# Optimization experiments

Hardware: AMD Instinct MI355X
Metric: run time of the kernel (lower is better)

## Reference

```python
import jax, jax.numpy as jnp
import numpy as np

N = 20000          # total nodes across batched graphs
E_REL = 60000      # edges per relation type (3 relation types)
N_CLASSES = 32
NUM_GRAPHS = 64
HEADS = 8
OUT_CH = 48
FUSED = 384        # 3 * 128 fused node feature dim
EPS = 1e-5         # PyG LayerNorm eps
NEG_SLOPE = 0.2    # RGATConv leaky_relu slope
NUM_ITERS = 2


def setup_inputs() -> dict:
    key = jax.random.key(0)
    ks = iter(jax.random.split(key, 48))

    def nrm(shape, scale=0.05):
        return jax.random.normal(next(ks), shape, jnp.float32) * scale

    inp = {}
    inp["x_visual"] = jax.random.normal(next(ks), (N, 1024), jnp.float32)
    inp["x_geom"] = jax.random.normal(next(ks), (N, 6), jnp.float32)
    inp["x_prior"] = jax.random.uniform(next(ks), (N, N_CLASSES + 1), jnp.float32)
    inp["edge_index_overlap"] = jax.random.randint(next(ks), (2, E_REL), 0, N)
    inp["edge_index_arch"] = jax.random.randint(next(ks), (2, E_REL), 0, N)
    inp["edge_index_spatial"] = jax.random.randint(next(ks), (2, E_REL), 0, N)
    inp["batch"] = jnp.sort(jax.random.randint(next(ks), (N,), 0, NUM_GRAPHS))
    # encoders: Linear -> ReLU -> PyG LayerNorm(graph mode, batch=None)
    inp["vis_W"] = nrm((1024, 128)); inp["vis_b"] = jnp.zeros((128,), jnp.float32)
    inp["vis_lnw"] = jnp.ones((128,), jnp.float32); inp["vis_lnb"] = jnp.zeros((128,), jnp.float32)
    inp["geo_W"] = nrm((6, 128)); inp["geo_b"] = jnp.zeros((128,), jnp.float32)
    inp["geo_lnw"] = jnp.ones((128,), jnp.float32); inp["geo_lnb"] = jnp.zeros((128,), jnp.float32)
    inp["pri_W"] = nrm((N_CLASSES + 1, 128)); inp["pri_b"] = jnp.zeros((128,), jnp.float32)
    inp["pri_lnw"] = jnp.ones((128,), jnp.float32); inp["pri_lnb"] = jnp.zeros((128,), jnp.float32)
    # RGATConv params: weight (R, in, H*O), q/k (H*O, H*dim) with dim=1, bias (H*O)
    for i in (1, 2):
        inp[f"rgat{i}_W"] = nrm((3, FUSED, HEADS * OUT_CH))
        inp[f"rgat{i}_q"] = nrm((HEADS * OUT_CH, HEADS))
        inp[f"rgat{i}_k"] = nrm((HEADS * OUT_CH, HEADS))
        inp[f"rgat{i}_bias"] = jnp.zeros((HEADS * OUT_CH,), jnp.float32)
        inp[f"n{i}_w"] = jnp.ones((FUSED,), jnp.float32)
        inp[f"n{i}_b"] = jnp.zeros((FUSED,), jnp.float32)
    inp["cls_W1"] = nrm((FUSED, 128)); inp["cls_b1"] = jnp.zeros((128,), jnp.float32)
    inp["cls_W2"] = nrm((128, N_CLASSES)); inp["cls_b2"] = jnp.zeros((N_CLASSES,), jnp.float32)
    return inp


def _encoder(x, W, b, lnw, lnb):
    # Linear -> ReLU -> PyG LayerNorm(mode='graph', batch=None): scalar mean/std
    h = jax.nn.relu(x @ W + b)
    h = h - h.mean()
    h = h / (h.std() + EPS)
    return h * lnw + lnb


def _graph_layernorm(x, batch, w, b):
    # PyG LayerNorm(mode='graph') with batch vector: normalize per graph over nodes*channels
    cnt = jax.ops.segment_sum(jnp.ones((x.shape[0],), x.dtype), batch, NUM_GRAPHS)
    norm = jnp.clip(cnt, 1.0, None) * x.shape[-1]
    mean = jax.ops.segment_sum(x, batch, NUM_GRAPHS).sum(-1) / norm
    xc = x - mean[batch][:, None]
    var = jax.ops.segment_sum(xc * xc, batch, NUM_GRAPHS).sum(-1) / norm
    out = xc / jnp.sqrt(var + EPS)[batch][:, None]
    return out * w + b


def _rgat(x, src, dst, etype, W, q, k, bias):
    # RGATConv: additive self-attention, across-relation softmax, concat heads, sum aggr
    n = x.shape[0]
    xr = jnp.einsum('nf,rfo->rno', x, W)          # per-relation node transform (R,N,H*O)
    outi = xr[etype, dst]                          # (E, H*O) transformed dst features
    outj = xr[etype, src]                          # (E, H*O) transformed src features
    alpha = jax.nn.leaky_relu(outi @ q + outj @ k, NEG_SLOPE)  # (E, H)
    amax = jax.ops.segment_max(alpha, dst, n)
    amax = jnp.where(jnp.isfinite(amax), amax, 0.0)
    ex = jnp.exp(alpha - amax[dst])
    den = jax.ops.segment_sum(ex, dst, n)
    a = ex / (den[dst] + 1e-16)                    # per-dst-node softmax over all relations
    msg = (a[:, :, None] * outj.reshape(-1, HEADS, OUT_CH)).reshape(-1, HEADS * OUT_CH)
    return jax.ops.segment_sum(msg, dst, n) + bias


def reference(x_visual, x_geom, x_prior, edge_index_overlap, edge_index_arch,
              edge_index_spatial, batch, vis_W, vis_b, vis_lnw, vis_lnb,
              geo_W, geo_b, geo_lnw, geo_lnb, pri_W, pri_b, pri_lnw, pri_lnb,
              rgat1_W, rgat1_q, rgat1_k, rgat1_bias, n1_w, n1_b,
              rgat2_W, rgat2_q, rgat2_k, rgat2_bias, n2_w, n2_b,
              cls_W1, cls_b1, cls_W2, cls_b2):
    ei = jnp.concatenate([edge_index_overlap, edge_index_arch, edge_index_spatial], axis=1)
    src, dst = ei[0], ei[1]
    etype = jnp.concatenate([jnp.full((E_REL,), r, jnp.int32) for r in range(3)])

    h_vis = _encoder(x_visual, vis_W, vis_b, vis_lnw, vis_lnb)
    h_geo = _encoder(x_geom, geo_W, geo_b, geo_lnw, geo_lnb)

    cur_prior = x_prior
    logits = None
    for t in range(NUM_ITERS):
        h_pri = _encoder(cur_prior, pri_W, pri_b, pri_lnw, pri_lnb)
        h0 = jnp.concatenate([h_vis, h_geo, h_pri], axis=-1)  # (N, 384)
        h1 = jax.nn.elu(_rgat(h0, src, dst, etype, rgat1_W, rgat1_q, rgat1_k, rgat1_bias)) + h0
        h1 = _graph_layernorm(h1, batch, n1_w, n1_b)
        h2 = jax.nn.elu(_rgat(h1, src, dst, etype, rgat2_W, rgat2_q, rgat2_k, rgat2_bias)) + h1
        h2 = _graph_layernorm(h2, batch, n2_w, n2_b)
        logits = jax.nn.relu(h2 @ cls_W1 + cls_b1) @ cls_W2 + cls_b2  # dropout off (eval)
        if t < NUM_ITERS - 1:
            probs = jax.nn.softmax(logits, axis=-1)
            cur_prior = jnp.concatenate([probs, probs.max(-1, keepdims=True)], axis=-1)
    return logits
```

## Files before the change

kernel.cpp:

```cpp
#include <hip/hip_runtime.h>
#include <hip/hip_bf16.h>

#define Nn 20000
#define EREL 60000
#define ETOT 180000
#define NG 64
#define FD 384
#define EPS 1e-5f

typedef unsigned short u16;
typedef unsigned int u32;
typedef __attribute__((ext_vector_type(8))) short s8v;
typedef __attribute__((ext_vector_type(4))) float f4v;

static inline int cdiv(int a, int b) { return (a + b - 1) / b; }

__device__ inline u16 f2b(float f) {
    __hip_bfloat16 h = __float2bfloat16(f);
    union { __hip_bfloat16 b; u16 u; } c; c.b = h; return c.u;
}
__device__ inline float b2f(u16 u) {
    union { __hip_bfloat16 b; u16 u; } c; c.u = u; return __bfloat162float(c.b);
}

template<bool WLO>
__global__ void tsplit_k(const float* __restrict__ W, u16* __restrict__ hi,
                         u16* __restrict__ lo, int K, int N, int total)
{
    int idx = blockIdx.x * 256 + threadIdx.x;
    if (idx >= total) return;
    int kn = K * N;
    int b = idx / kn, rem = idx - b * kn;
    int k = rem / N, n = rem - k * N;
    float v = W[idx];
    u16 h = f2b(v);
    int o = b * kn + n * K + k;
    hi[o] = h;
    if (WLO) lo[o] = f2b(v - b2f(h));
}

__global__ __launch_bounds__(256) void w2_k(const float* __restrict__ W0,
    const float* __restrict__ q0, const float* __restrict__ k0,
    const float* __restrict__ W1, const float* __restrict__ q1, const float* __restrict__ k1,
    u16* __restrict__ hi, u16* __restrict__ lo)
{
    int row = blockIdx.x * 4 + (threadIdx.x >> 6);
    int lane = threadIdx.x & 63;
    if (row >= 2304) return;
    int kin = row % 384;
    int lr3 = row / 384;
    int L = lr3 / 3, r = lr3 - L * 3;
    const float* W = (L ? W1 : W0) + ((size_t)r * 384 + kin) * 384;
    const float* qm = L ? q1 : q0;
    const float* km = L ? k1 : k0;
    float pq[16] = {};
    #pragma unroll
    for (int j = 0; j < 6; j++) {
        int d = lane + 64 * j;
        float x = W[d];
        #pragma unroll
        for (int h = 0; h < 8; h++) {
            pq[h]     = fmaf(x, qm[d * 8 + h], pq[h]);
            pq[8 + h] = fmaf(x, km[d * 8 + h], pq[8 + h]);
        }
    }
    #pragma unroll
    for (int o = 32; o; o >>= 1) {
        #pragma unroll
        for (int h = 0; h < 16; h++) pq[h] += __shfl_down(pq[h], o);
    }
    if (lane == 0) {
        #pragma unroll
        for (int c = 0; c < 16; c++) {
            u16 hh = f2b(pq[c]);
            size_t o = ((size_t)L * 48 + r * 16 + c) * 384 + kin;
            hi[o] = hh; lo[o] = f2b(pq[c] - b2f(hh));
        }
    }
}

__global__ __launch_bounds__(256) void enc_gemm_k(const float* __restrict__ x, int K,
    const float* __restrict__ W, const float* __restrict__ bias,
    u16* __restrict__ out, float* __restrict__ stats)
{
    __shared__ float Wl[33 * 128];
    __shared__ float bl[128];
    __shared__ float red[8];
    int t = threadIdx.x;
    for (int i = t; i < K * 128; i += 256) Wl[i] = W[i];
    if (t < 128) bl[t] = bias[t];
    __syncthreads();
    int wid = t >> 6, lane = t & 63;
    float s1 = 0.f, s2 = 0.f;
    for (int rr = 0; rr < 8; rr++) {
        int n = blockIdx.x * 32 + wid * 8 + rr;
        if (n >= Nn) break;
        float xv = (lane < K) ? x[(size_t)n * K + lane] : 0.f;
        float a0 = 0.f, a1 = 0.f;
        for (int k = 0; k < K; k++) {
            float xk = __shfl(xv, k);
            a0 = fmaf(xk, Wl[k * 128 + 2 * lane], a0);
            a1 = fmaf(xk, Wl[k * 128 + 2 * lane + 1], a1);
        }
        a0 = fmaxf(a0 + bl[2 * lane], 0.f);
        a1 = fmaxf(a1 + bl[2 * lane + 1], 0.f);
        ((u32*)(out + (size_t)n * FD))[lane] = (u32)f2b(a0) | ((u32)f2b(a1) << 16);
        s1 += a0 + a1; s2 += a0 * a0 + a1 * a1;
    }
    #pragma unroll
    for (int o = 32; o; o >>= 1) { s1 += __shfl_down(s1, o); s2 += __shfl_down(s2, o); }
    if (lane == 0) { red[wid] = s1; red[4 + wid] = s2; }
    __syncthreads();
    if (t == 0) atomicAdd(&stats[0], red[0] + red[1] + red[2] + red[3]);
    if (t == 1) atomicAdd(&stats[1], red[4] + red[5] + red[6] + red[7]);
}

#define USEI(i) ((i) < 2 || ((i) >= 4 && (i) < 6) || (TERMS >= 2 && ((i) == 2 || (i) == 3)) || (TERMS >= 3 && (i) >= 6))
template<bool BIAS, bool RELU, bool STATS, bool OB16, int TERMS, bool SWZ, bool AF32>
__global__ __launch_bounds__(256) void mgemm_k(
    const u16* __restrict__ Ahi, const u16* __restrict__ Alo, const float* __restrict__ Af,
    const u16* __restrict__ Bhi, const u16* __restrict__ Blo,
    const float* __restrict__ bias, void* __restrict__ Cv,
    int M, int K, int ldc, int bstride, float* __restrict__ stats)
{
    __shared__ u16 lds[4 * 128 * 32];
    __shared__ float red[256];
    const int t = threadIdx.x;
    int brow, bcol, z;
    if (SWZ) {
        int d = blockIdx.x;
        int xcd = d & 7, s = d >> 3;
        int row = xcd + 8 * (s / 9);
        int c = s % 9;
        brow = row * 128;
        if (brow >= M) return;
        bcol = (c % 3) * 128;
        z = c / 3;
    } else {
        brow = blockIdx.x * 128; bcol = blockIdx.y * 128; z = blockIdx.z;
    }
    Bhi += (size_t)z * bstride;
    Blo += (size_t)z * bstride;
    float* Cf = OB16 ? nullptr : (float*)Cv + (size_t)z * M * ldc;
    u16*   Ch = OB16 ? (u16*)Cv + (size_t)z * M * ldc : nullptr;

    const int r0 = t >> 2, sl = t & 3;
    const int rA0 = min(brow + r0, M - 1);
    const int rA1 = min(brow + r0 + 64, M - 1);
    const u16* gsrc[8];
    gsrc[0] = Ahi + (size_t)rA0 * K + sl * 8;
    gsrc[1] = Ahi + (size_t)rA1 * K + sl * 8;
    gsrc[2] = Alo + (size_t)rA0 * K + sl * 8;
    gsrc[3] = Alo + (size_t)rA1 * K + sl * 8;
    gsrc[4] = Bhi + (size_t)(bcol + r0) * K + sl * 8;
    gsrc[5] = Bhi + (size_t)(bcol + r0 + 64) * K + sl * 8;
    gsrc[6] = Blo + (size_t)(bcol + r0) * K + sl * 8;
    gsrc[7] = Blo + (size_t)(bcol + r0 + 64) * K + sl * 8;
    const float* afsrc[2];
    if (AF32) {
        afsrc[0] = Af + (size_t)rA0 * K + sl * 8;
        afsrc[1] = Af + (size_t)rA1 * K + sl * 8;
    }
    const int swz = (sl ^ (r0 & 3)) << 3;
    int ldst[8];
    #pragma unroll
    for (int i = 0; i < 8; i++) {
        int tile = i >> 1, row = r0 + 64 * (i & 1);
        ldst[i] = tile * 4096 + row * 32 + swz;
    }

    const int l = t & 63, w = t >> 6;
    const int wr = (w >> 1) * 64, wc = (w & 1) * 64;
    const int lr = l & 15, kq = l >> 4;

    f4v acc[4][4] = {};
    const int NK = K >> 5;

    #define LDA32(i, ko) ({ \
        float4 f0_ = *(const float4*)(afsrc[i] + (ko)); \
        float4 f1_ = *(const float4*)(afsrc[i] + (ko) + 4); \
        s8v r_; \
        r_[0] = (short)f2b(f0_.x); r_[1] = (short)f2b(f0_.y); \
        r_[2] = (short)f2b(f0_.z); r_[3] = (short)f2b(f0_.w); \
        r_[4] = (short)f2b(f1_.x); r_[5] = (short)f2b(f1_.y); \
        r_[6] = (short)f2b(f1_.z); r_[7] = (short)f2b(f1_.w); \
        r_; })

    s8v stg[8];
    #pragma unroll
    for (int i = 0; i < 8; i++) {
        if (AF32 && i < 2) stg[i] = LDA32(i, 0);
        else if (!(AF32 && i < 2) && USEI(i)) stg[i] = *(const s8v*)gsrc[i];
    }

    for (int kc = 0; kc < NK; kc++) {
        if (kc) __syncthreads();
        #pragma unroll
        for (int i = 0; i < 8; i++) if (USEI(i)) *(s8v*)(lds + ldst[i]) = stg[i];
        __syncthreads();
        if (kc + 1 < NK) {
            const int ko = (kc + 1) * 32;
            #pragma unroll
            for (int i = 0; i < 8; i++) {
                if (AF32 && i < 2) stg[i] = LDA32(i, ko);
                else if (!(AF32 && i < 2) && USEI(i)) stg[i] = *(const s8v*)(gsrc[i] + ko);
            }
        }
        #define LDR(T, row) (*(const s8v*)(lds + (T) * 4096 + (row) * 32 + ((kq ^ ((row) & 3)) << 3)))
        s8v bh[4], bl[4];
        #pragma unroll
        for (int tn = 0; tn < 4; tn++) {
            int rb = wc + tn * 16 + lr;
            bh[tn] = LDR(2, rb);
            if (TERMS >= 3) bl[tn] = LDR(3, rb);
        }
        #pragma unroll
        for (int tm = 0; tm < 4; tm++) {
            int ra = wr + tm * 16 + lr;
            s8v ah = LDR(0, ra);
            s8v al;
            if (TERMS >= 2) al = LDR(1, ra);
            #pragma unroll
            for (int tn = 0; tn < 4; tn++) {
                acc[tm][tn] = __builtin_amdgcn_mfma_f32_16x16x32_bf16(ah, bh[tn], acc[tm][tn], 0, 0, 0);
                if (TERMS >= 2)
                    acc[tm][tn] = __builtin_amdgcn_mfma_f32_16x16x32_bf16(al, bh[tn], acc[tm][tn], 0, 0, 0);
                if (TERMS >= 3)
                    acc[tm][tn] = __builtin_amdgcn_mfma_f32_16x16x32_bf16(ah, bl[tn], acc[tm][tn], 0, 0, 0);
            }
        }
        #undef LDR
    }
    #undef LDA32

    float s1 = 0.f, s2 = 0.f;
    #pragma unroll
    for (int tm = 0; tm < 4; tm++) {
        #pragma unroll
        for (int rg = 0; rg < 4; rg++) {
            int row = brow + wr + tm * 16 + kq * 4 + rg;
            if (row < M) {
                #pragma unroll
                for (int tn = 0; tn < 4; tn++) {
                    int col = bcol + wc + tn * 16 + lr;
                    float v = acc[tm][tn][rg];
                    if (BIAS) v += bias[col];
                    if (RELU) v = fmaxf(v, 0.f);
                    if (OB16) Ch[(size_t)row * ldc + col] = f2b(v);
                    else      Cf[(size_t)row * ldc + col] = v;
                    if (STATS) { s1 += v; s2 += v * v; }
                }
            }
        }
    }
    if (STATS) {
        __syncthreads();
        red[t] = s1; __syncthreads();
        for (int o = 128; o; o >>= 1) { if (t < o) red[t] += red[t + o]; __syncthreads(); }
        if (t == 0) atomicAdd(&stats[0], red[0]);
        __syncthreads();
        red[t] = s2; __syncthreads();
        for (int o = 128; o; o >>= 1) { if (t < o) red[t] += red[t + o]; __syncthreads(); }
        if (t == 0) atomicAdd(&stats[1], red[0]);
    }
}
#undef USEI

__global__ __launch_bounds__(256) void projh_k(const u16* __restrict__ hs,
    const u16* __restrict__ w2hi, const u16* __restrict__ w2lo, float* __restrict__ qik)
{
    __shared__ u16 a_lds[128 * 32];
    __shared__ u16 b_lds[2][48 * 392];
    int t = threadIdx.x;
    int brow = blockIdx.x * 128;

    for (int i = t; i < 2304; i += 256) {
        int col = i / 48, c8 = (i - col * 48) * 8;
        *(s8v*)&b_lds[0][col * 392 + c8] = *(const s8v*)(w2hi + col * 384 + c8);
        *(s8v*)&b_lds[1][col * 392 + c8] = *(const s8v*)(w2lo + col * 384 + c8);
    }

    int ar = t >> 1, sl0 = (t & 1) * 2;
    int grow = min(brow + ar, Nn - 1);
    const u16* asrc = hs + (size_t)grow * FD;
    int adst0 = ar * 32 + ((sl0 ^ (ar & 3)) << 3);
    int adst1 = ar * 32 + (((sl0 + 1) ^ (ar & 3)) << 3);

    int l = t & 63, w = t >> 6;
    int lr = l & 15, kq = l >> 4;
    f4v acc[2][3] = {};

    s8v stg0 = *(const s8v*)(asrc + sl0 * 8);
    s8v stg1 = *(const s8v*)(asrc + sl0 * 8 + 8);
    for (int kc = 0; kc < 12; kc++) {
        if (kc) __syncthreads();
        *(s8v*)&a_lds[adst0] = stg0;
        *(s8v*)&a_lds[adst1] = stg1;
        __syncthreads();
        if (kc + 1 < 12) {
            int ko = (kc + 1) * 32 + sl0 * 8;
            stg0 = *(const s8v*)(asrc + ko);
            stg1 = *(const s8v*)(asrc + ko + 8);
        }
        s8v bh[3], bl[3];
        #pragma unroll
        for (int cf = 0; cf < 3; cf++) {
            bh[cf] = *(const s8v*)&b_lds[0][(cf * 16 + lr) * 392 + kc * 32 + kq * 8];
            bl[cf] = *(const s8v*)&b_lds[1][(cf * 16 + lr) * 392 + kc * 32 + kq * 8];
        }
        #pragma unroll
        for (int rf = 0; rf < 2; rf++) {
            int rr = w * 32 + rf * 16 + lr;
            s8v a = *(const s8v*)&a_lds[rr * 32 + ((kq ^ (rr & 3)) << 3)];
            #pragma unroll
            for (int cf = 0; cf < 3; cf++) {
                acc[rf][cf] = __builtin_amdgcn_mfma_f32_16x16x32_bf16(a, bh[cf], acc[rf][cf], 0, 0, 0);
                acc[rf][cf] = __builtin_amdgcn_mfma_f32_16x16x32_bf16(a, bl[cf], acc[rf][cf], 0, 0, 0);
            }
        }
    }
    #pragma unroll
    for (int rf = 0; rf < 2; rf++)
        #pragma unroll
        for (int cf = 0; cf < 3; cf++)
            #pragma unroll
            for (int rg = 0; rg < 4; rg++) {
                int row = brow + w * 32 + rf * 16 + kq * 4 + rg;
                if (row < Nn) qik[(size_t)row * 48 + cf * 16 + lr] = acc[rf][cf][rg];
            }
}

template<bool BIAS, bool RELU>
__global__ __launch_bounds__(256) void sgemm_k(
    const float* __restrict__ A, const float* __restrict__ B,
    const float* __restrict__ bias, float* __restrict__ C,
    int M, int K, int N, int ldc)
{
    const int BK = 16;
    __shared__ float As[16][65];
    __shared__ float Bs[16][64];
    int tid = threadIdx.x;
    int tx = tid & 15, ty = tid >> 4;
    int brow = blockIdx.x * 64, bcol = blockIdx.y * 64;
    float acc[4][4] = {};
    for (int k0 = 0; k0 < K; k0 += BK) {
        #pragma unroll
        for (int i = 0; i < 4; i++) {
            int e = tid + 256 * i;
            int ar = e >> 4, ak = e & 15;
            int gr = brow + ar, gk = k0 + ak;
            As[ak][ar] = (gr < M && gk < K) ? A[(size_t)gr * K + gk] : 0.f;
            int bk = e >> 6, bn = e & 63;
            int gbk = k0 + bk, gbn = bcol + bn;
            Bs[bk][bn] = (gbk < K && gbn < N) ? B[(size_t)gbk * N + gbn] : 0.f;
        }
        __syncthreads();
        #pragma unroll
        for (int k = 0; k < BK; k++) {
            float ra[4], rb[4];
            #pragma unroll
            for (int i = 0; i < 4; i++) ra[i] = As[k][ty * 4 + i];
            #pragma unroll
            for (int j = 0; j < 4; j++) rb[j] = Bs[k][tx * 4 + j];
            #pragma unroll
            for (int i = 0; i < 4; i++)
                #pragma unroll
                for (int j = 0; j < 4; j++)
                    acc[i][j] = fmaf(ra[i], rb[j], acc[i][j]);
        }
        __syncthreads();
    }
    #pragma unroll
    for (int i = 0; i < 4; i++) {
        int row = brow + ty * 4 + i;
        #pragma unroll
        for (int j = 0; j < 4; j++) {
            int col = bcol + tx * 4 + j;
            if (row < M && col < N) {
                float v = acc[i][j];
                if (BIAS) v += bias[col];
                if (RELU) v = v > 0.f ? v : 0.f;
                C[(size_t)row * ldc + col] = v;
            }
        }
    }
}

__global__ __launch_bounds__(256) void enc_norm_k(const u16* __restrict__ H,
                           const float* __restrict__ w, const float* __restrict__ b,
                           const float* __restrict__ stats, float cntinv, u16* __restrict__ hi)
{
    int i = blockIdx.x * 256 + threadIdx.x;
    if (i >= Nn * 32) return;
    int n = i >> 5, c4 = i & 31;
    float m = stats[0] * cntinv;
    float var = stats[1] * cntinv - m * m;
    float s = 1.f / (sqrtf(fmaxf(var, 0.f)) + EPS);
    float4 wv = ((const float4*)w)[c4];
    float4 bv = ((const float4*)b)[c4];
    uint2 yv = ((const uint2*)(H + (size_t)n * FD))[c4];
    ushort4 hh;
    hh.x = f2b((b2f((u16)(yv.x & 0xffffu)) - m) * s * wv.x + bv.x);
    hh.y = f2b((b2f((u16)(yv.x >> 16))     - m) * s * wv.y + bv.y);
    hh.z = f2b((b2f((u16)(yv.y & 0xffffu)) - m) * s * wv.z + bv.z);
    hh.w = f2b((b2f((u16)(yv.y >> 16))     - m) * s * wv.w + bv.w);
    ((ushort4*)(hi + (size_t)n * FD))[c4] = hh;
}

__global__ void edge_count_k(const int* __restrict__ e0, const int* __restrict__ e1,
                             const int* __restrict__ e2, int* __restrict__ cnt)
{
    int e = blockIdx.x * 256 + threadIdx.x;
    if (e >= ETOT) return;
    int r = e / EREL, i = e - r * EREL;
    const int* ei = (r == 0) ? e0 : (r == 1) ? e1 : e2;
    atomicAdd(&cnt[ei[EREL + i]], 1);
}

__global__ void edge_fill_k(const int* __restrict__ e0, const int* __restrict__ e1,
                            const int* __restrict__ e2, int* __restrict__ cursor,
                            int* __restrict__ eidx)
{
    int e = blockIdx.x * 256 + threadIdx.x;
    if (e >= ETOT) return;
    int r = e / EREL, i = e - r * EREL;
    const int* ei = (r == 0) ? e0 : (r == 1) ? e1 : e2;
    int src = ei[i], dst = ei[EREL + i];
    int pos = atomicAdd(&cursor[dst], 1);
    eidx[pos] = src | (r << 24);
}

__global__ __launch_bounds__(1024) void scan_k(const int* __restrict__ cnt,
                                               int* __restrict__ rowptr, int* __restrict__ cursor)
{
    __shared__ int wsum[16], wpre[16];
    __shared__ int carry, tot;
    int t = threadIdx.x, lane = t & 63, wid = t >> 6;
    if (t == 0) carry = 0;
    __syncthreads();
    for (int base = 0; base < Nn; base += 1024) {
        int i = base + t;
        int v = (i < Nn) ? cnt[i] : 0;
        int s = v;
        #pragma unroll
        for (int o = 1; o < 64; o <<= 1) {
            int x = __shfl_up(s, o);
            if (lane >= o) s += x;
        }
        if (lane == 63) wsum[wid] = s;
        __syncthreads();
        if (t < 16) {
            int wv = wsum[t];
            int ws = wv;
            #pragma unroll
            for (int o = 1; o < 16; o <<= 1) {
                int x = __shfl_up(ws, o);
                if (t >= o) ws += x;
            }
            wpre[t] = ws - wv;
            if (t == 15) tot = ws;
        }
        __syncthreads();
        if (i < Nn) {
            int ex = carry + wpre[wid] + s - v;
            rowptr[i] = ex; cursor[i] = ex;
        }
        __syncthreads();
        if (t == 0) carry += tot;
    }
    __syncthreads();
    if (t == 0) rowptr[Nn] = carry;
}

__global__ __launch_bounds__(256) void gcount_k(const int* __restrict__ batch, int* __restrict__ gcnt)
{
    __shared__ int bins[NG];
    int t = threadIdx.x;
    if (t < NG) bins[t] = 0;
    __syncthreads();
    int n = blockIdx.x * 256 + t;
    if (n < Nn) atomicAdd(&bins[batch[n]], 1);
    __syncthreads();
    if (t < NG && bins[t]) atomicAdd(&gcnt[t], bins[t]);
}

__global__ __launch_bounds__(256) void aggr_k(const u16* __restrict__ xr,
    const float* __restrict__ qik, const int* __restrict__ rowptr, const int* __restrict__ eidx,
    const float* __restrict__ bias, const u16* __restrict__ hinb,
    const int* __restrict__ batch, u16* __restrict__ outb,
    float* __restrict__ gsum, float* __restrict__ gsq)
{
    __shared__ float ls[NG], lq[NG];
    int t = threadIdx.x;
    if (t < NG) { ls[t] = 0.f; lq[t] = 0.f; }
    __syncthreads();
    int node = blockIdx.x * 4 + (t >> 6);
    int lane = t & 63;
    int e0 = rowptr[node], e1 = rowptr[node + 1];
    int hd = lane >> 3;
    float qv = (lane < 48) ? qik[(size_t)node * 48 + lane] : 0.f;
    float den = 0.f;
    float acc[6] = {};

    int e = e0;
    while (e + 4 <= e1) {
        int p0 = eidx[e], p1 = eidx[e + 1], p2 = eidx[e + 2], p3 = eidx[e + 3];
        int n0 = p0 & 0xFFFFFF, et0 = p0 >> 24;
        int n1 = p1 & 0xFFFFFF, et1 = p1 >> 24;
        int n2 = p2 & 0xFFFFFF, et2 = p2 >> 24;
        int n3 = p3 & 0xFFFFFF, et3 = p3 >> 24;
        float kv0 = (lane < 8) ? qik[(size_t)n0 * 48 + et0 * 16 + 8 + lane] : 0.f;
        float kv1 = (lane < 8) ? qik[(size_t)n1 * 48 + et1 * 16 + 8 + lane] : 0.f;
        float kv2 = (lane < 8) ? qik[(size_t)n2 * 48 + et2 * 16 + 8 + lane] : 0.f;
        float kv3 = (lane < 8) ? qik[(size_t)n3 * 48 + et3 * 16 + 8 + lane] : 0.f;
        const u32* r0 = (const u32*)(xr + ((size_t)et0 * Nn + n0) * FD);
        const u32* r1 = (const u32*)(xr + ((size_t)et1 * Nn + n1) * FD);
        const u32* r2 = (const u32*)(xr + ((size_t)et2 * Nn + n2) * FD);
        const u32* r3 = (const u32*)(xr + ((size_t)et3 * Nn + n3) * FD);
        u32 u0[3], u1[3], u2[3], u3[3];
        #pragma unroll
        for (int j = 0; j < 3; j++) u0[j] = r0[lane * 3 + j];
        #pragma unroll
        for (int j = 0; j < 3; j++) u1[j] = r1[lane * 3 + j];
        #pragma unroll
        for (int j = 0; j < 3; j++) u2[j] = r2[lane * 3 + j];
        #pragma unroll
        for (int j = 0; j < 3; j++) u3[j] = r3[lane * 3 + j];
        float qq0 = __shfl(qv, et0 * 16 + (lane & 7));
        float qq1 = __shfl(qv, et1 * 16 + (lane & 7));
        float qq2 = __shfl(qv, et2 * 16 + (lane & 7));
        float qq3 = __shfl(qv, et3 * 16 + (lane & 7));
        float ex0 = 0.f, ex1 = 0.f, ex2 = 0.f, ex3 = 0.f;
        if (lane < 8) {
            float a0 = qq0 + kv0; a0 = (a0 > 0.f) ? a0 : 0.2f * a0; ex0 = __expf(a0);
            float a1 = qq1 + kv1; a1 = (a1 > 0.f) ? a1 : 0.2f * a1; ex1 = __expf(a1);
            float a2 = qq2 + kv2; a2 = (a2 > 0.f) ? a2 : 0.2f * a2; ex2 = __expf(a2);
            float a3 = qq3 + kv3; a3 = (a3 > 0.f) ? a3 : 0.2f * a3; ex3 = __expf(a3);
        }
        den += ex0 + ex1 + ex2 + ex3;
        float w0 = __shfl(ex0, hd), w1 = __shfl(ex1, hd);
        float w2 = __shfl(ex2, hd), w3 = __shfl(ex3, hd);
        #pragma unroll
        for (int j = 0; j < 3; j++) {
            acc[2*j]   = fmaf(w0, __uint_as_float(u0[j] << 16), acc[2*j]);
            acc[2*j+1] = fmaf(w0, __uint_as_float(u0[j] & 0xffff0000u), acc[2*j+1]);
            acc[2*j]   = fmaf(w1, __uint_as_float(u1[j] << 16), acc[2*j]);
            acc[2*j+1] = fmaf(w1, __uint_as_float(u1[j] & 0xffff0000u), acc[2*j+1]);
            acc[2*j]   = fmaf(w2, __uint_as_float(u2[j] << 16), acc[2*j]);
            acc[2*j+1] = fmaf(w2, __uint_as_float(u2[j] & 0xffff0000u), acc[2*j+1]);
            acc[2*j]   = fmaf(w3, __uint_as_float(u3[j] << 16), acc[2*j]);
            acc[2*j+1] = fmaf(w3, __uint_as_float(u3[j] & 0xffff0000u), acc[2*j+1]);
        }
        e += 4;
    }
    for (; e < e1; e++) {
        int p = eidx[e];
        int sn = p & 0xFFFFFF, et = p >> 24;
        float kv = (lane < 8) ? qik[(size_t)sn * 48 + et * 16 + 8 + lane] : 0.f;
        const u32* rr = (const u32*)(xr + ((size_t)et * Nn + sn) * FD);
        u32 u[3];
        #pragma unroll
        for (int j = 0; j < 3; j++) u[j] = rr[lane * 3 + j];
        float qq = __shfl(qv, et * 16 + (lane & 7));
        float ex = 0.f;
        if (lane < 8) { float a = qq + kv; a = (a > 0.f) ? a : 0.2f * a; ex = __expf(a); }
        den += ex;
        float wv_ = __shfl(ex, hd);
        #pragma unroll
        for (int j = 0; j < 3; j++) {
            acc[2*j]   = fmaf(wv_, __uint_as_float(u[j] << 16), acc[2*j]);
            acc[2*j+1] = fmaf(wv_, __uint_as_float(u[j] & 0xffff0000u), acc[2*j+1]);
        }
    }

    float dh = __shfl(den, hd);
    float rcp = 1.f / (dh + 1e-16f);
    const u32* hp = (const u32*)(hinb + (size_t)node * FD);
    u32* op = (u32*)(outb + (size_t)node * FD);
    float s1 = 0.f, s2 = 0.f;
    #pragma unroll
    for (int j = 0; j < 3; j++) {
        int c = lane * 6 + 2 * j;
        float2 bv = *(const float2*)(bias + c);
        u32 hb = hp[lane * 3 + j];
        float vx = acc[2*j] * rcp + bv.x;
        float vy = acc[2*j+1] * rcp + bv.y;
        vx = (vx > 0.f) ? vx : expm1f(vx);
        vy = (vy > 0.f) ? vy : expm1f(vy);
        vx += b2f((u16)(hb & 0xffffu));
        vy += b2f((u16)(hb >> 16));
        op[lane * 3 + j] = (u32)f2b(vx) | ((u32)f2b(vy) << 16);
        s1 += vx + vy; s2 += vx * vx + vy * vy;
    }
    #pragma unroll
    for (int o = 32; o; o >>= 1) { s1 += __shfl_down(s1, o); s2 += __shfl_down(s2, o); }
    int g = batch[node];
    if (lane == 0) { atomicAdd(&ls[g], s1); atomicAdd(&lq[g], s2); }
    __syncthreads();
    if (t < NG && (ls[t] != 0.f || lq[t] != 0.f)) {
        atomicAdd(&gsum[t], ls[t]);
        atomicAdd(&gsq[t], lq[t]);
    }
}

template<bool WLO>
__global__ __launch_bounds__(256) void gnorm_split_k(const u16* __restrict__ yb,
    const int* __restrict__ batch, const float* __restrict__ gsum, const float* __restrict__ gsq,
    const int* __restrict__ gcnt, const float* __restrict__ w, const float* __restrict__ b,
    u16* __restrict__ hi, u16* __restrict__ lo)
{
    int i = blockIdx.x * 256 + threadIdx.x;
    if (i >= Nn * (FD / 4)) return;
    int n = i / 96;
    int c4 = i - n * 96;
    int g = batch[n];
    float norm = fmaxf((float)gcnt[g], 1.f) * (float)FD;
    float m = gsum[g] / norm;
    float var = gsq[g] / norm - m * m;
    float rstd = rsqrtf(var + EPS);
    float4 wv = ((const float4*)w)[c4];
    float4 bv = ((const float4*)b)[c4];
    uint2 yv = ((const uint2*)yb)[i];
    float v0 = (b2f((u16)(yv.x & 0xffffu)) - m) * rstd * wv.x + bv.x;
    float v1 = (b2f((u16)(yv.x >> 16))     - m) * rstd * wv.y + bv.y;
    float v2 = (b2f((u16)(yv.y & 0xffffu)) - m) * rstd * wv.z + bv.z;
    float v3 = (b2f((u16)(yv.y >> 16))     - m) * rstd * wv.w + bv.w;
    ushort4 hh;
    hh.x = f2b(v0); hh.y = f2b(v1); hh.z = f2b(v2); hh.w = f2b(v3);
    ((ushort4*)hi)[i] = hh;
    if (WLO) {
        ushort4 ll;
        ll.x = f2b(v0 - b2f(hh.x));
        ll.y = f2b(v1 - b2f(hh.y));
        ll.z = f2b(v2 - b2f(hh.z));
        ll.w = f2b(v3 - b2f(hh.w));
        ((ushort4*)lo)[i] = ll;
    }
}

__global__ void softmax_prior_k(const float* __restrict__ logits, float* __restrict__ prior)
{
    int n = blockIdx.x * 8 + (threadIdx.x >> 5);
    int l = threadIdx.x & 31;
    if (n >= Nn) return;
    float v = logits[n * 32 + l];
    float m = v;
    #pragma unroll
    for (int o = 16; o; o >>= 1) m = fmaxf(m, __shfl_xor(m, o, 32));
    float e = __expf(v - m);
    float s = e;
    #pragma unroll
    for (int o = 16; o; o >>= 1) s += __shfl_xor(s, o, 32);
    prior[(size_t)n * 33 + l] = e / s;
    if (l == 0) prior[(size_t)n * 33 + 32] = 1.f / s;
}

extern "C" void kernel_launch(void* const* d_in, const int* in_sizes, int n_in,
                              void* d_out, int out_size, void* d_ws, size_t ws_size,
                              hipStream_t stream)
{
    const float* x_visual = (const float*)d_in[0];
    const float* x_geom   = (const float*)d_in[1];
    const float* x_prior  = (const float*)d_in[2];
    const int* ei0   = (const int*)d_in[3];
    const int* ei1   = (const int*)d_in[4];
    const int* ei2   = (const int*)d_in[5];
    const int* batch = (const int*)d_in[6];
    const float* vis_W = (const float*)d_in[7];  const float* vis_b = (const float*)d_in[8];
    const float* vis_lnw = (const float*)d_in[9]; const float* vis_lnb = (const float*)d_in[10];
    const float* geo_W = (const float*)d_in[11]; const float* geo_b = (const float*)d_in[12];
    const float* geo_lnw = (const float*)d_in[13]; const float* geo_lnb = (const float*)d_in[14];
    const float* pri_W = (const float*)d_in[15]; const float* pri_b = (const float*)d_in[16];
    const float* pri_lnw = (const float*)d_in[17]; const float* pri_lnb = (const float*)d_in[18];
    const float* rgat_W[2]    = { (const float*)d_in[19], (const float*)d_in[25] };
    const float* rgat_q[2]    = { (const float*)d_in[20], (const float*)d_in[26] };
    const float* rgat_kk[2]   = { (const float*)d_in[21], (const float*)d_in[27] };
    const float* rgat_bias[2] = { (const float*)d_in[22], (const float*)d_in[28] };
    const float* ln_w[2]      = { (const float*)d_in[23], (const float*)d_in[29] };
    const float* ln_b[2]      = { (const float*)d_in[24], (const float*)d_in[30] };
    const float* cls_W1 = (const float*)d_in[31]; const float* cls_b1 = (const float*)d_in[32];
    const float* cls_W2 = (const float*)d_in[33]; const float* cls_b2 = (const float*)d_in[34];
    float* OUT = (float*)d_out;

    float* ws = (float*)d_ws;
    float* XRreg = ws;
    u16*   XR16  = (u16*)XRreg;
    float* HCAT  = XRreg + (size_t)3 * Nn * FD;
    u16*   HENC  = (u16*)HCAT;
    float* HA    = HCAT + (size_t)Nn * FD;
    float* HB    = HA + (size_t)Nn * FD;
    float* PRIOR = HB + (size_t)Nn * FD;
    float* QIK   = PRIOR + (size_t)Nn * 33;
    u16* HS0_HI  = (u16*)(QIK + (size_t)Nn * 48);
    u16* HS0_LO  = HS0_HI + (size_t)Nn * FD;
    u16* HS1_HI  = HS0_LO + (size_t)Nn * FD;
    u16* HS1_LO  = HS1_HI + (size_t)Nn * FD;
    u16* RW_HI   = HS1_LO + (size_t)Nn * FD;
    u16* RW_LO   = RW_HI + (size_t)2 * 3 * 384 * 384;
    u16* VW_HI   = RW_LO + (size_t)2 * 3 * 384 * 384;
    u16* VW_LO   = VW_HI + (size_t)128 * 1024;
    u16* CW_HI   = VW_LO + (size_t)128 * 1024;
    u16* CW_LO   = CW_HI + (size_t)128 * 384;
    u16* W2_HI   = CW_LO + (size_t)128 * 384;
    u16* W2_LO   = W2_HI + (size_t)2 * 48 * 384;
    float* GS    = (float*)(W2_LO + (size_t)2 * 48 * 384);
    float* STATS = GS + 512;
    int* CNT    = (int*)(STATS + 8);
    int* ROWPTR = CNT + Nn;
    int* CURSOR = ROWPTR + Nn + 1;
    int* EIDX   = CURSOR + Nn;
    int* GCNT   = EIDX + ETOT;
    float* CLSH = XRreg;
    u16* HS2_HI = (u16*)(XRreg + (size_t)12 * 1000 * 1000);
    u16* HS2_LO = HS2_HI + (size_t)Nn * FD;
    u16* YB0 = (u16*)HA;
    u16* YB1 = (u16*)HB;

    hipMemsetAsync(CNT, 0, Nn * sizeof(int), stream);
    edge_count_k<<<cdiv(ETOT, 256), 256, 0, stream>>>(ei0, ei1, ei2, CNT);
    scan_k<<<1, 1024, 0, stream>>>(CNT, ROWPTR, CURSOR);
    edge_fill_k<<<cdiv(ETOT, 256), 256, 0, stream>>>(ei0, ei1, ei2, CURSOR, EIDX);
    hipMemsetAsync(GCNT, 0, 64 * sizeof(int), stream);
    gcount_k<<<cdiv(Nn, 256), 256, 0, stream>>>(batch, GCNT);
    hipMemsetAsync(GS, 0, 520 * sizeof(float), stream);

    tsplit_k<false><<<cdiv(3 * 384 * 384, 256), 256, 0, stream>>>(rgat_W[0], RW_HI, RW_LO, 384, 384, 3 * 384 * 384);
    tsplit_k<false><<<cdiv(3 * 384 * 384, 256), 256, 0, stream>>>(rgat_W[1], RW_HI + 3 * 384 * 384, RW_LO, 384, 384, 3 * 384 * 384);
    tsplit_k<false><<<cdiv(1024 * 128, 256), 256, 0, stream>>>(vis_W, VW_HI, VW_LO, 1024, 128, 1024 * 128);
    tsplit_k<true><<<cdiv(384 * 128, 256), 256, 0, stream>>>(cls_W1, CW_HI, CW_LO, 384, 128, 384 * 128);
    w2_k<<<576, 256, 0, stream>>>(rgat_W[0], rgat_q[0], rgat_kk[0],
                                  rgat_W[1], rgat_q[1], rgat_kk[1], W2_HI, W2_LO);

    const int MB = cdiv(Nn, 128);
    const int XRBLK = 160 * 9;
    const float cinv = 1.f / ((float)Nn * 128.f);

    mgemm_k<true, true, true, true, 1, false, true><<<dim3(MB, 1, 1), 256, 0, stream>>>(
        nullptr, nullptr, x_visual, VW_HI, VW_LO, vis_b, HENC, Nn, 1024, FD, 0, STATS + 0);
    enc_norm_k<<<cdiv(Nn * 32, 256), 256, 0, stream>>>(HENC, vis_lnw, vis_lnb, STATS + 0, cinv, HS0_HI);

    enc_gemm_k<<<cdiv(Nn, 32), 256, 0, stream>>>(x_geom, 6, geo_W, geo_b, HENC + 128, STATS + 2);
    enc_norm_k<<<cdiv(Nn * 32, 256), 256, 0, stream>>>(HENC + 128, geo_lnw, geo_lnb, STATS + 2, cinv, HS0_HI + 128);

    for (int t = 0; t < 2; t++) {
        const float* pin = t ? PRIOR : x_prior;
        enc_gemm_k<<<cdiv(Nn, 32), 256, 0, stream>>>(pin, 33, pri_W, pri_b, HENC + 256, STATS + 4 + 2 * t);
        enc_norm_k<<<cdiv(Nn * 32, 256), 256, 0, stream>>>(HENC + 256, pri_lnw, pri_lnb, STATS + 4 + 2 * t, cinv, HS0_HI + 256);

        for (int L = 0; L < 2; L++) {
            const u16* ahi = L ? HS1_HI : HS0_HI;
            u16* yout = L ? YB1 : YB0;
            float* gsum = GS + (t * 2 + L) * 128;
            mgemm_k<false, false, false, true, 1, true, false><<<dim3(XRBLK, 1, 1), 256, 0, stream>>>(
                ahi, ahi, nullptr, RW_HI + (size_t)L * 3 * 384 * 384, RW_LO,
                nullptr, XR16, Nn, 384, FD, 384 * 384, nullptr);
            projh_k<<<MB, 256, 0, stream>>>(ahi,
                W2_HI + (size_t)L * 48 * 384, W2_LO + (size_t)L * 48 * 384, QIK);
            aggr_k<<<cdiv(Nn, 4), 256, 0, stream>>>(XR16, QIK, ROWPTR, EIDX, rgat_bias[L],
                                                    ahi, batch, yout, gsum, gsum + 64);
            if (L == 0)
                gnorm_split_k<false><<<cdiv(Nn * 96, 256), 256, 0, stream>>>(
                    YB0, batch, gsum, gsum + 64, GCNT, ln_w[0], ln_b[0], HS1_HI, HS1_LO);
            else
                gnorm_split_k<true><<<cdiv(Nn * 96, 256), 256, 0, stream>>>(
                    YB1, batch, gsum, gsum + 64, GCNT, ln_w[1], ln_b[1], HS2_HI, HS2_LO);
        }

        mgemm_k<true, true, false, false, 3, false, false><<<dim3(MB, 1, 1), 256, 0, stream>>>(
            HS2_HI, HS2_LO, nullptr, CW_HI, CW_LO, cls_b1, CLSH, Nn, 384, 128, 0, nullptr);
        sgemm_k<true, false><<<dim3(cdiv(Nn, 64), 1, 1), 256, 0, stream>>>(
            CLSH, cls_W2, cls_b2, OUT, Nn, 128, 32, 32);

        if (t == 0)
            softmax_prior_k<<<cdiv(Nn, 8), 256, 0, stream>>>(OUT, PRIOR);
    }
}
```

Measured before the change: 738.1 us.

## Fuse classifier MLP and softmax-prior into one MFMA kernel, drop lo split

```diff
diff --git a/kernel.cpp b/kernel.cpp
--- a/kernel.cpp
+++ b/kernel.cpp
@@ -266,6 +266,127 @@
 }
 #undef USEI
 
+template<bool DOSM>
+__global__ __launch_bounds__(256) void mcls_k(
+    const u16* __restrict__ A, const u16* __restrict__ Bh, const float* __restrict__ b1,
+    const u16* __restrict__ w2hi, const u16* __restrict__ w2lo, const float* __restrict__ b2,
+    float* __restrict__ outp, float* __restrict__ prior)
+{
+    __shared__ u16 lds[128 * 132];
+    __shared__ u16 w2lds[2][32 * 132];
+    const int t = threadIdx.x;
+    const int brow = blockIdx.x * 128;
+
+    for (int i = t; i < 512; i += 256) {
+        int row = i >> 4, c8 = (i & 15) * 8;
+        *(s8v*)&w2lds[0][row * 132 + c8] = *(const s8v*)(w2hi + row * 128 + c8);
+        *(s8v*)&w2lds[1][row * 132 + c8] = *(const s8v*)(w2lo + row * 128 + c8);
+    }
+
+    const int r0 = t >> 2, sl = t & 3;
+    const int rA0 = min(brow + r0, Nn - 1);
+    const int rA1 = min(brow + r0 + 64, Nn - 1);
+    const u16* gA0 = A + (size_t)rA0 * FD + sl * 8;
+    const u16* gA1 = A + (size_t)rA1 * FD + sl * 8;
+    const u16* gB0 = Bh + (size_t)r0 * FD + sl * 8;
+    const u16* gB1 = Bh + (size_t)(r0 + 64) * FD + sl * 8;
+    const int swz = (sl ^ (r0 & 3)) << 3;
+    const int la0 = r0 * 32 + swz, la1 = (r0 + 64) * 32 + swz;
+    const int lb0 = 2 * 4096 + r0 * 32 + swz, lb1 = 2 * 4096 + (r0 + 64) * 32 + swz;
+
+    const int l = t & 63, w = t >> 6;
+    const int wr = (w >> 1) * 64, wc = (w & 1) * 64;
+    const int lr = l & 15, kq = l >> 4;
+
+    f4v acc[4][4] = {};
+    s8v sA0 = *(const s8v*)gA0, sA1 = *(const s8v*)gA1;
+    s8v sB0 = *(const s8v*)gB0, sB1 = *(const s8v*)gB1;
+    for (int kc = 0; kc < 12; kc++) {
+        if (kc) __syncthreads();
+        *(s8v*)(lds + la0) = sA0; *(s8v*)(lds + la1) = sA1;
+        *(s8v*)(lds + lb0) = sB0; *(s8v*)(lds + lb1) = sB1;
+        __syncthreads();
+        if (kc + 1 < 12) {
+            int ko = (kc + 1) * 32;
+            sA0 = *(const s8v*)(gA0 + ko); sA1 = *(const s8v*)(gA1 + ko);
+            sB0 = *(const s8v*)(gB0 + ko); sB1 = *(const s8v*)(gB1 + ko);
+        }
+        #define LDR(T, row) (*(const s8v*)(lds + (T) * 4096 + (row) * 32 + ((kq ^ ((row) & 3)) << 3)))
+        s8v bh[4];
+        #pragma unroll
+        for (int tn = 0; tn < 4; tn++) bh[tn] = LDR(2, wc + tn * 16 + lr);
+        #pragma unroll
+        for (int tm = 0; tm < 4; tm++) {
+            s8v ah = LDR(0, wr + tm * 16 + lr);
+            #pragma unroll
+            for (int tn = 0; tn < 4; tn++)
+                acc[tm][tn] = __builtin_amdgcn_mfma_f32_16x16x32_bf16(ah, bh[tn], acc[tm][tn], 0, 0, 0);
+        }
+        #undef LDR
+    }
+    __syncthreads();
+
+    #pragma unroll
+    for (int tm = 0; tm < 4; tm++)
+        #pragma unroll
+        for (int rg = 0; rg < 4; rg++) {
+            int row = wr + tm * 16 + kq * 4 + rg;
+            #pragma unroll
+            for (int tn = 0; tn < 4; tn++) {
+                int col = wc + tn * 16 + lr;
+                lds[row * 132 + col] = f2b(fmaxf(acc[tm][tn][rg] + b1[col], 0.f));
+            }
+        }
+    __syncthreads();
+
+    f4v a2[2][2] = {};
+    #pragma unroll
+    for (int ks = 0; ks < 4; ks++) {
+        #pragma unroll
+        for (int rf = 0; rf < 2; rf++) {
+            int ar = w * 32 + rf * 16 + lr;
+            s8v av = *(const s8v*)&lds[ar * 132 + ks * 32 + kq * 8];
+            #pragma unroll
+            for (int cf = 0; cf < 2; cf++) {
+                s8v bhv = *(const s8v*)&w2lds[0][(cf * 16 + lr) * 132 + ks * 32 + kq * 8];
+                s8v blv = *(const s8v*)&w2lds[1][(cf * 16 + lr) * 132 + ks * 32 + kq * 8];
+                a2[rf][cf] = __builtin_amdgcn_mfma_f32_16x16x32_bf16(av, bhv, a2[rf][cf], 0, 0, 0);
+                a2[rf][cf] = __builtin_amdgcn_mfma_f32_16x16x32_bf16(av, blv, a2[rf][cf], 0, 0, 0);
+            }
+        }
+    }
+    #pragma unroll
+    for (int rf = 0; rf < 2; rf++) {
+        #pragma unroll
+        for (int rg = 0; rg < 4; rg++) {
+            int grow = brow + w * 32 + rf * 16 + kq * 4 + rg;
+            float v0 = a2[rf][0][rg] + b2[lr];
+            float v1 = a2[rf][1][rg] + b2[16 + lr];
+            if (grow < Nn) {
+                outp[(size_t)grow * 32 + lr] = v0;
+                outp[(size_t)grow * 32 + 16 + lr] = v1;
+            }
+            if (DOSM) {
+                float m = fmaxf(v0, v1);
+                m = fmaxf(m, __shfl_xor(m, 1));
+                m = fmaxf(m, __shfl_xor(m, 2));
+                m = fmaxf(m, __shfl_xor(m, 4));
+                m = fmaxf(m, __shfl_xor(m, 8));
+                float e0 = __expf(v0 - m), e1 = __expf(v1 - m);
+                float s = e0 + e1;
+                s += __shfl_xor(s, 1); s += __shfl_xor(s, 2);
+                s += __shfl_xor(s, 4); s += __shfl_xor(s, 8);
+                if (grow < Nn) {
+                    float rs = 1.f / s;
+                    prior[(size_t)grow * 33 + lr] = e0 * rs;
+                    prior[(size_t)grow * 33 + 16 + lr] = e1 * rs;
+                    if (lr == 0) prior[(size_t)grow * 33 + 32] = rs;
+                }
+            }
+        }
+    }
+}
+
 __global__ __launch_bounds__(256) void projh_k(const u16* __restrict__ hs,
     const u16* __restrict__ w2hi, const u16* __restrict__ w2lo, float* __restrict__ qik)
 {
@@ -328,62 +449,6 @@
                 int row = brow + w * 32 + rf * 16 + kq * 4 + rg;
                 if (row < Nn) qik[(size_t)row * 48 + cf * 16 + lr] = acc[rf][cf][rg];
             }
-}
-
-template<bool BIAS, bool RELU>
-__global__ __launch_bounds__(256) void sgemm_k(
-    const float* __restrict__ A, const float* __restrict__ B,
-    const float* __restrict__ bias, float* __restrict__ C,
-    int M, int K, int N, int ldc)
-{
-    const int BK = 16;
-    __shared__ float As[16][65];
-    __shared__ float Bs[16][64];
-    int tid = threadIdx.x;
-    int tx = tid & 15, ty = tid >> 4;
-    int brow = blockIdx.x * 64, bcol = blockIdx.y * 64;
-    float acc[4][4] = {};
-    for (int k0 = 0; k0 < K; k0 += BK) {
-        #pragma unroll
-        for (int i = 0; i < 4; i++) {
-            int e = tid + 256 * i;
-            int ar = e >> 4, ak = e & 15;
-            int gr = brow + ar, gk = k0 + ak;
-            As[ak][ar] = (gr < M && gk < K) ? A[(size_t)gr * K + gk] : 0.f;
-            int bk = e >> 6, bn = e & 63;
-            int gbk = k0 + bk, gbn = bcol + bn;
-            Bs[bk][bn] = (gbk < K && gbn < N) ? B[(size_t)gbk * N + gbn] : 0.f;
-        }
-        __syncthreads();
-        #pragma unroll
-        for (int k = 0; k < BK; k++) {
-            float ra[4], rb[4];
-            #pragma unroll
-            for (int i = 0; i < 4; i++) ra[i] = As[k][ty * 4 + i];
-            #pragma unroll
-            for (int j = 0; j < 4; j++) rb[j] = Bs[k][tx * 4 + j];
-            #pragma unroll
-            for (int i = 0; i < 4; i++)
-                #pragma unroll
-                for (int j = 0; j < 4; j++)
-                    acc[i][j] = fmaf(ra[i], rb[j], acc[i][j]);
-        }
-        __syncthreads();
-    }
-    #pragma unroll
-    for (int i = 0; i < 4; i++) {
-        int row = brow + ty * 4 + i;
-        #pragma unroll
-        for (int j = 0; j < 4; j++) {
-            int col = bcol + tx * 4 + j;
-            if (row < M && col < N) {
-                float v = acc[i][j];
-                if (BIAS) v += bias[col];
-                if (RELU) v = v > 0.f ? v : 0.f;
-                C[(size_t)row * ldc + col] = v;
-            }
-        }
-    }
 }
 
 __global__ __launch_bounds__(256) void enc_norm_k(const u16* __restrict__ H,
@@ -603,11 +668,10 @@
     }
 }
 
-template<bool WLO>
 __global__ __launch_bounds__(256) void gnorm_split_k(const u16* __restrict__ yb,
     const int* __restrict__ batch, const float* __restrict__ gsum, const float* __restrict__ gsq,
     const int* __restrict__ gcnt, const float* __restrict__ w, const float* __restrict__ b,
-    u16* __restrict__ hi, u16* __restrict__ lo)
+    u16* __restrict__ hi)
 {
     int i = blockIdx.x * 256 + threadIdx.x;
     if (i >= Nn * (FD / 4)) return;
@@ -621,38 +685,12 @@
     float4 wv = ((const float4*)w)[c4];
     float4 bv = ((const float4*)b)[c4];
     uint2 yv = ((const uint2*)yb)[i];
-    float v0 = (b2f((u16)(yv.x & 0xffffu)) - m) * rstd * wv.x + bv.x;
-    float v1 = (b2f((u16)(yv.x >> 16))     - m) * rstd * wv.y + bv.y;
-    float v2 = (b2f((u16)(yv.y & 0xffffu)) - m) * rstd * wv.z + bv.z;
-    float v3 = (b2f((u16)(yv.y >> 16))     - m) * rstd * wv.w + bv.w;
     ushort4 hh;
-    hh.x = f2b(v0); hh.y = f2b(v1); hh.z = f2b(v2); hh.w = f2b(v3);
+    hh.x = f2b((b2f((u16)(yv.x & 0xffffu)) - m) * rstd * wv.x + bv.x);
+    hh.y = f2b((b2f((u16)(yv.x >> 16))     - m) * rstd * wv.y + bv.y);
+    hh.z = f2b((b2f((u16)(yv.y & 0xffffu)) - m) * rstd * wv.z + bv.z);
+    hh.w = f2b((b2f((u16)(yv.y >> 16))     - m) * rstd * wv.w + bv.w);
     ((ushort4*)hi)[i] = hh;
-    if (WLO) {
-        ushort4 ll;
-        ll.x = f2b(v0 - b2f(hh.x));
-        ll.y = f2b(v1 - b2f(hh.y));
-        ll.z = f2b(v2 - b2f(hh.z));
-        ll.w = f2b(v3 - b2f(hh.w));
-        ((ushort4*)lo)[i] = ll;
-    }
-}
-
-__global__ void softmax_prior_k(const float* __restrict__ logits, float* __restrict__ prior)
-{
-    int n = blockIdx.x * 8 + (threadIdx.x >> 5);
-    int l = threadIdx.x & 31;
-    if (n >= Nn) return;
-    float v = logits[n * 32 + l];
-    float m = v;
-    #pragma unroll
-    for (int o = 16; o; o >>= 1) m = fmaxf(m, __shfl_xor(m, o, 32));
-    float e = __expf(v - m);
-    float s = e;
-    #pragma unroll
-    for (int o = 16; o; o >>= 1) s += __shfl_xor(s, o, 32);
-    prior[(size_t)n * 33 + l] = e / s;
-    if (l == 0) prior[(size_t)n * 33 + 32] = 1.f / s;
 }
 
 extern "C" void kernel_launch(void* const* d_in, const int* in_sizes, int n_in,
@@ -700,8 +738,9 @@
     u16* VW_HI   = RW_LO + (size_t)2 * 3 * 384 * 384;
     u16* VW_LO   = VW_HI + (size_t)128 * 1024;
     u16* CW_HI   = VW_LO + (size_t)128 * 1024;
-    u16* CW_LO   = CW_HI + (size_t)128 * 384;
-    u16* W2_HI   = CW_LO + (size_t)128 * 384;
+    u16* W2T_HI  = CW_HI + (size_t)128 * 384;
+    u16* W2T_LO  = W2T_HI + (size_t)32 * 128;
+    u16* W2_HI   = W2T_LO + (size_t)32 * 128;
     u16* W2_LO   = W2_HI + (size_t)2 * 48 * 384;
     float* GS    = (float*)(W2_LO + (size_t)2 * 48 * 384);
     float* STATS = GS + 512;
@@ -710,9 +749,7 @@
     int* CURSOR = ROWPTR + Nn + 1;
     int* EIDX   = CURSOR + Nn;
     int* GCNT   = EIDX + ETOT;
-    float* CLSH = XRreg;
     u16* HS2_HI = (u16*)(XRreg + (size_t)12 * 1000 * 1000);
-    u16* HS2_LO = HS2_HI + (size_t)Nn * FD;
     u16* YB0 = (u16*)HA;
     u16* YB1 = (u16*)HB;
 
@@ -727,7 +764,8 @@
     tsplit_k<false><<<cdiv(3 * 384 * 384, 256), 256, 0, stream>>>(rgat_W[0], RW_HI, RW_LO, 384, 384, 3 * 384 * 384);
     tsplit_k<false><<<cdiv(3 * 384 * 384, 256), 256, 0, stream>>>(rgat_W[1], RW_HI + 3 * 384 * 384, RW_LO, 384, 384, 3 * 384 * 384);
     tsplit_k<false><<<cdiv(1024 * 128, 256), 256, 0, stream>>>(vis_W, VW_HI, VW_LO, 1024, 128, 1024 * 128);
-    tsplit_k<true><<<cdiv(384 * 128, 256), 256, 0, stream>>>(cls_W1, CW_HI, CW_LO, 384, 128, 384 * 128);
+    tsplit_k<false><<<cdiv(384 * 128, 256), 256, 0, stream>>>(cls_W1, CW_HI, nullptr, 384, 128, 384 * 128);
+    tsplit_k<true><<<cdiv(128 * 32, 256), 256, 0, stream>>>(cls_W2, W2T_HI, W2T_LO, 128, 32, 128 * 32);
     w2_k<<<576, 256, 0, stream>>>(rgat_W[0], rgat_q[0], rgat_kk[0],
                                   rgat_W[1], rgat_q[1], rgat_kk[1], W2_HI, W2_LO);
 
@@ -750,6 +788,7 @@
         for (int L = 0; L < 2; L++) {
             const u16* ahi = L ? HS1_HI : HS0_HI;
             u16* yout = L ? YB1 : YB0;
+            u16* snorm = L ? HS2_HI : HS1_HI;
             float* gsum = GS + (t * 2 + L) * 128;
             mgemm_k<false, false, false, true, 1, true, false><<<dim3(XRBLK, 1, 1), 256, 0, stream>>>(
                 ahi, ahi, nullptr, RW_HI + (size_t)L * 3 * 384 * 384, RW_LO,
@@ -758,20 +797,15 @@
                 W2_HI + (size_t)L * 48 * 384, W2_LO + (size_t)L * 48 * 384, QIK);
             aggr_k<<<cdiv(Nn, 4), 256, 0, stream>>>(XR16, QIK, ROWPTR, EIDX, rgat_bias[L],
                                                     ahi, batch, yout, gsum, gsum + 64);
-            if (L == 0)
-                gnorm_split_k<false><<<cdiv(Nn * 96, 256), 256, 0, stream>>>(
-                    YB0, batch, gsum, gsum + 64, GCNT, ln_w[0], ln_b[0], HS1_HI, HS1_LO);
-            else
-                gnorm_split_k<true><<<cdiv(Nn * 96, 256), 256, 0, stream>>>(
-                    YB1, batch, gsum, gsum + 64, GCNT, ln_w[1], ln_b[1], HS2_HI, HS2_LO);
-        }
-
-        mgemm_k<true, true, false, false, 3, false, false><<<dim3(MB, 1, 1), 256, 0, stream>>>(
-            HS2_HI, HS2_LO, nullptr, CW_HI, CW_LO, cls_b1, CLSH, Nn, 384, 128, 0, nullptr);
-        sgemm_k<true, false><<<dim3(cdiv(Nn, 64), 1, 1), 256, 0, stream>>>(
-            CLSH, cls_W2, cls_b2, OUT, Nn, 128, 32, 32);
+            gnorm_split_k<<<cdiv(Nn * 96, 256), 256, 0, stream>>>(
+                yout, batch, gsum, gsum + 64, GCNT, ln_w[L], ln_b[L], snorm);
+        }
 
         if (t == 0)
-            softmax_prior_k<<<cdiv(Nn, 8), 256, 0, stream>>>(OUT, PRIOR);
-    }
-}
+            mcls_k<true><<<dim3(MB, 1, 1), 256, 0, stream>>>(
+                HS2_HI, CW_HI, cls_b1, W2T_HI, W2T_LO, cls_b2, OUT, PRIOR);
+        else
+            mcls_k<false><<<dim3(MB, 1, 1), 256, 0, stream>>>(
+                HS2_HI, CW_HI, cls_b1, W2T_HI, W2T_LO, cls_b2, OUT, nullptr);
+    }
+}
```

After: 679.7 us. 1.09x faster.
